# Kernel tuning notes

Hardware: AMD Instinct MI355X
Metric: run time of the kernel (lower is better)

## Reference

```python
import jax, jax.numpy as jnp
import numpy as np

B, T, IN_DIM, OUT_DIM = 1024, 64, 8, 2
H, K, HIDDEN = 3, 5, 256
LOG_STD_MIN, LOG_STD_MAX = -20.0, 2.0


def setup_inputs() -> dict:
    key = jax.random.key(0)
    ks = jax.random.split(key, 12)
    def lin(k, fan_in, fan_out):
        b = 1.0 / np.sqrt(fan_in)
        return jax.random.uniform(k, (fan_in, fan_out), jnp.float32, -b, b)
    inp = {
        'state': jax.random.normal(ks[0], (B, T, IN_DIM), jnp.float32),
        'noise': jax.random.normal(ks[1], (B, T, OUT_DIM), jnp.float32),
        'Wq': lin(ks[2], IN_DIM, K * H),
        'Wk': lin(ks[3], K, K * H),
        'Wv': lin(ks[4], K, K * H),
        'W1': lin(ks[5], K * H + IN_DIM, HIDDEN),
        'b1': jnp.zeros((HIDDEN,), jnp.float32),
        'W2': lin(ks[6], HIDDEN, HIDDEN),
        'b2': jnp.zeros((HIDDEN,), jnp.float32),
        'Wmu': jax.random.uniform(ks[7], (HIDDEN, OUT_DIM), jnp.float32, -0.003, 0.003),
        'bmu': jax.random.uniform(ks[8], (OUT_DIM,), jnp.float32, -0.003, 0.003),
        'Wls': jax.random.uniform(ks[9], (HIDDEN, OUT_DIM), jnp.float32, -0.003, 0.003),
        'bls': jax.random.uniform(ks[10], (OUT_DIM,), jnp.float32, -0.003, 0.003),
    }
    return inp


# static off-diagonal neighbor indices: row i -> all j != i
_OFFDIAG = np.array([[j for j in range(T) if j != i] for i in range(T)], dtype=np.int32)


def _forward(state, noise, Wq, Wk, Wv, W1, b1, W2, b2, Wmu, bmu, Wls, bls):
    b, t, _ = state.shape
    # rel[b,i,j] = state[b,j,:4] - state[b,i,:4]
    rel4 = state[:, None, :, 0:4] - state[:, :, None, 0:4]          # [b,t,t,4] (x,y,vx,vy)
    x_comp = rel4[..., 0::2]                                         # [x, vx]
    y_comp = rel4[..., 1::2]                                         # [y, vy]
    ang = (-state[:, :, 7] + 0.5 * jnp.pi)[:, None, :, None]         # varies with j (own-ref of key agent)
    c, s = jnp.cos(ang), jnp.sin(ang)
    xn = x_comp * c - y_comp * s                                     # [x', vx']
    yn = x_comp * s + y_comp * c                                     # [y', vy']
    rel = jnp.stack([xn[..., 0], yn[..., 0], xn[..., 1], yn[..., 1]], axis=-1)  # [b,t,t,4]
    # drop self-pairs (diagonal) -> [b,t,t-1,4]
    idx = jnp.asarray(_OFFDIAG)
    rel_od = rel[:, jnp.arange(t)[:, None], idx]
    r = jnp.sqrt(rel_od[..., 0] ** 2 + rel_od[..., 1] ** 2)[..., None]   # [b,t,t-1,1]
    r_trans = jax.nn.sigmoid(1.0 - 5.0 * (r - 0.2))                       # 1/(1+exp(-1+5(r-0.2)))
    rel_n = jnp.concatenate([rel_od[..., 0:2] / r, rel_od[..., 2:4], r_trans], axis=-1)  # [b,t,t-1,5]
    h, k = H, K
    q = (state @ Wq).reshape(b, t, h, k)                              # [b,t,h,k]
    keys = (rel_n @ Wk).reshape(b, t, t - 1, h, k)                    # [b,t,n,h,k]
    vals = (rel_n @ Wv).reshape(b, t, t - 1, h, k)
    scores = jnp.einsum('btnhk,bthk->bthn', keys, q) / jnp.sqrt(jnp.float32(k))
    w = jax.nn.softmax(scores, axis=-1)                               # over t-1 neighbors
    att = jnp.einsum('bthn,btnhk->bthk', w, vals).reshape(b, t, h * k)
    x = jnp.concatenate([att, state], axis=-1)
    x = jax.nn.relu(x @ W1 + b1)
    x = jax.nn.relu(x @ W2 + b2)
    mu = jnp.tanh(x @ Wmu + bmu)
    log_std = jnp.tanh(x @ Wls + bls)
    log_std = LOG_STD_MIN + 0.5 * (LOG_STD_MAX - LOG_STD_MIN) * (log_std + 1.0)
    std = jnp.exp(log_std)
    z = mu + std * noise                                              # rsample with explicit noise
    action = jnp.tanh(z)
    # Normal(mu,std).log_prob(z) with (z-mu)/std == noise
    log_prob = -0.5 * noise ** 2 - log_std - 0.5 * jnp.log(2.0 * jnp.pi)
    log_prob = log_prob - jnp.log(1.0 - action ** 2 + 1e-7)
    log_prob = jnp.sum(log_prob, axis=-1, keepdims=True)
    return action, log_prob


def reference(state, noise, Wq, Wk, Wv, W1, b1, W2, b2, Wmu, bmu, Wls, bls):
    return _forward(state, noise, Wq, Wk, Wv, W1, b1, W2, b2, Wmu, bmu, Wls, bls)
```

## Files before the change

### kernel.cpp

```cpp
#include <hip/hip_runtime.h>
#include <math.h>

#define NROWS 65536

typedef short bf16x8 __attribute__((ext_vector_type(8)));
typedef float f32x4  __attribute__((ext_vector_type(4)));
typedef float f32x2  __attribute__((ext_vector_type(2)));
typedef unsigned int u32x2 __attribute__((ext_vector_type(2)));

__device__ __forceinline__ unsigned short f2bf(float x){
    unsigned int u = __float_as_uint(x);
    u += 0x7FFFu + ((u >> 16) & 1u);
    return (unsigned short)(u >> 16);
}
__device__ __forceinline__ unsigned int pkbf(float lo, float hi){
    unsigned int r;
    asm("v_cvt_pk_bf16_f32 %0, %1, %2" : "=v"(r) : "v"(lo), "v"(hi));
    return r;
}
__device__ __forceinline__ f32x2 sp2(float x){ return (f32x2){x, x}; }

template<int CTRL, int RM>
__device__ __forceinline__ float dpp_add(float v){
    int m = __builtin_amdgcn_update_dpp(0, __float_as_int(v), CTRL, RM, 0xF, 1);
    return v + __int_as_float(m);
}
__device__ __forceinline__ float bfly8_add(float v){
    v = dpp_add<0xB1, 0xF>(v);
    v = dpp_add<0x4E, 0xF>(v);
    v = dpp_add<0x141, 0xF>(v);
    return v;
}
__device__ __forceinline__ float red4_lq(float v){
    v += __int_as_float(__builtin_amdgcn_ds_swizzle(__float_as_int(v), 0x401F));
    v += __shfl_xor(v, 32, 64);
    return v;
}
__device__ __forceinline__ float fast_tanh(float x){
    float e = __builtin_amdgcn_exp2f(x * 2.8853900817779268f);
    return 1.f - 2.f * __builtin_amdgcn_rcpf(e + 1.f);
}

__global__ __launch_bounds__(256) void prep_kernel(
    const float* __restrict__ W2, const float* __restrict__ W1,
    const float* __restrict__ Wq, const float* __restrict__ Wk,
    unsigned short* __restrict__ w2frag, unsigned short* __restrict__ w1frag,
    float* __restrict__ Cqk)
{
    const int bx = blockIdx.x, t = threadIdx.x;
    if (bx < 128){
        const int ct = bx >> 3, kk = bx & 7;
        #pragma unroll
        for (int s = 0; s < 2; ++s){
            int f = t * 2 + s;
            int lane = f >> 3, e = f & 7;
            int k = kk * 32 + (lane >> 4) * 8 + e;
            int c = ct * 16 + (lane & 15);
            w2frag[(size_t)(ct * 8 + kk) * 512 + f] = f2bf(W2[k * 256 + c]);
        }
    } else if (bx == 128){
        #pragma unroll
        for (int s = 0; s < 32; ++s){
            int flat = t * 32 + s;
            int ct = flat >> 9, r = flat & 511;
            int lane = r >> 3, e = r & 7;
            int k = (lane >> 4) * 8 + e;
            int c = ct * 16 + (lane & 15);
            w1frag[flat] = (k < 23) ? f2bf(W1[k * 256 + c]) : (unsigned short)0;
        }
    } else {
        if (t < 120){
            int h = t / 40, rem = t % 40, f = rem >> 3, d = rem & 7;
            float acc = 0.f;
            #pragma unroll
            for (int kk = 0; kk < 5; ++kk)
                acc += Wk[f * 15 + h * 5 + kk] * Wq[d * 15 + h * 5 + kk];
            Cqk[t] = acc * 0.64519834f;
        }
    }
}

__global__ __launch_bounds__(512, 4) void actor_kernel(
    const float* __restrict__ state, const float* __restrict__ noise,
    const float* __restrict__ Cqk,
    const float* __restrict__ Wv,
    const unsigned short* __restrict__ w1frag, const float* __restrict__ b1,
    const unsigned short* __restrict__ w2frag, const float* __restrict__ b2,
    const float* __restrict__ Wmu, const float* __restrict__ bmu,
    const float* __restrict__ Wls, const float* __restrict__ bls,
    float* __restrict__ action_out, float* __restrict__ logprob_out)
{
    __shared__ __align__(16) unsigned char uniA[64 * 264 * 2];
    float* sLDS  = (float*)uniA;
    float* pjLDS = sLDS + 576;
    float* qkLDS = pjLDS + 384;
    unsigned short* h1LDS = (unsigned short*)uniA;
    __shared__ __align__(16) unsigned short x0LDS[64 * 40];
    __shared__ __align__(16) float headLDS[8 * 64 * 4];

    const int t    = threadIdx.x;
    const int lane = t & 63;
    const int w    = t >> 6;
    const int lm   = lane & 15;
    const int lq   = lane >> 4;
    const int b    = blockIdx.x;

    {
        float v = state[(size_t)b * 512 + t];
        int r = t >> 3, c = t & 7;
        sLDS[r * 9 + c] = v;
        if (c < 4) pjLDS[(r & 31) * 12 + c * 2 + (r >> 5)] = v;

        if (t < 192){
            const int row = t & 63, h = t >> 6;
            f32x4 sA = *(const f32x4*)&state[(size_t)b * 512 + row * 8];
            f32x4 sB = *(const f32x4*)&state[(size_t)b * 512 + row * 8 + 4];
            #pragma unroll
            for (int f = 0; f < 5; ++f){
                const float* cp = &Cqk[(h * 5 + f) * 8];
                f32x4 cA = *(const f32x4*)cp;
                f32x4 cB = *(const f32x4*)(cp + 4);
                float acc = sA[0]*cA[0] + sA[1]*cA[1] + sA[2]*cA[2] + sA[3]*cA[3]
                          + sB[0]*cB[0] + sB[1]*cB[1] + sB[2]*cB[2] + sB[3]*cB[3];
                qkLDS[row * 20 + h * 5 + f] = acc;
            }
        } else if (w == 7){
            const int row = lane;
            float ang = 1.5707963267948966f - state[(size_t)b * 512 + row * 8 + 7];
            float sn, cs;
            __sincosf(ang, &sn, &cs);
            int base = (row & 31) * 12 + (row >> 5);
            pjLDS[base + 8]  = sn;
            pjLDS[base + 10] = cs;
        }
    }
    __syncthreads();

    {
        const int il = lane >> 3;
        const int js = lane & 7;
        const int i  = w * 8 + il;
        const float si0 = sLDS[i * 9 + 0], si1 = sLDS[i * 9 + 1];
        const float si2 = sLDS[i * 9 + 2], si3 = sLDS[i * 9 + 3];
        float qkv[16];
        *(f32x4*)&qkv[0]  = *(const f32x4*)&qkLDS[i * 20 + 0];
        *(f32x4*)&qkv[4]  = *(const f32x4*)&qkLDS[i * 20 + 4];
        *(f32x4*)&qkv[8]  = *(const f32x4*)&qkLDS[i * 20 + 8];
        *(f32x4*)&qkv[12] = *(const f32x4*)&qkLDS[i * 20 + 12];

        f32x2 s0 = {0.f,0.f}, s1 = {0.f,0.f}, s2 = {0.f,0.f};
        f32x2 g0[5], g1[5], g2[5];
        #pragma unroll
        for (int f = 0; f < 5; ++f){ g0[f] = sp2(0.f); g1[f] = sp2(0.f); g2[f] = sp2(0.f); }

        #pragma unroll
        for (int jj = 0; jj < 4; ++jj){
            const int jb = jj * 8 + js;
            const f32x2* pp = (const f32x2*)&pjLDS[jb * 12];
            f32x2 p0 = pp[0], p1 = pp[1], p2 = pp[2], p3 = pp[3];
            f32x2 sn = pp[4], cs = pp[5];
            f32x2 d0 = p0 - sp2(si0), d1 = p1 - sp2(si1);
            f32x2 d2 = p2 - sp2(si2), d3 = p3 - sp2(si3);
            f32x2 r2v = d0 * d0 + d1 * d1 + sp2(1e-30f);
            f32x2 xn0 = d0 * cs - d1 * sn, yn0 = d0 * sn + d1 * cs;
            f32x2 xn1 = d2 * cs - d3 * sn, yn1 = d2 * sn + d3 * cs;
            f32x2 inv_r;
            inv_r.x = __builtin_amdgcn_rsqf(r2v.x);
            inv_r.y = __builtin_amdgcn_rsqf(r2v.y);
            f32x2 rv  = r2v * inv_r;
            f32x2 arg = rv * sp2(7.2134752f) - sp2(2.8853901f);
            f32x2 f4;
            f4.x = __builtin_amdgcn_rcpf(1.f + __builtin_amdgcn_exp2f(arg.x));
            f4.y = __builtin_amdgcn_rcpf(1.f + __builtin_amdgcn_exp2f(arg.y));
            f32x2 f0 = xn0 * inv_r, f1 = yn0 * inv_r;
            f32x2 sc0 = f0*sp2(qkv[0])  + f1*sp2(qkv[1])  + xn1*sp2(qkv[2])  + yn1*sp2(qkv[3])  + f4*sp2(qkv[4]);
            f32x2 sc1 = f0*sp2(qkv[5])  + f1*sp2(qkv[6])  + xn1*sp2(qkv[7])  + yn1*sp2(qkv[8])  + f4*sp2(qkv[9]);
            f32x2 sc2 = f0*sp2(qkv[10]) + f1*sp2(qkv[11]) + xn1*sp2(qkv[12]) + yn1*sp2(qkv[13]) + f4*sp2(qkv[14]);
            f32x2 e0, e1, e2;
            e0.x = __builtin_amdgcn_exp2f(sc0.x);  e0.y = __builtin_amdgcn_exp2f(sc0.y);
            e1.x = __builtin_amdgcn_exp2f(sc1.x);  e1.y = __builtin_amdgcn_exp2f(sc1.y);
            e2.x = __builtin_amdgcn_exp2f(sc2.x);  e2.y = __builtin_amdgcn_exp2f(sc2.y);
            s0 += e0; s1 += e1; s2 += e2;
            g0[0] += e0*f0; g0[1] += e0*f1; g0[2] += e0*xn1; g0[3] += e0*yn1; g0[4] += e0*f4;
            g1[0] += e1*f0; g1[1] += e1*f1; g1[2] += e1*xn1; g1[3] += e1*yn1; g1[4] += e1*f4;
            g2[0] += e2*f0; g2[1] += e2*f1; g2[2] += e2*xn1; g2[3] += e2*yn1; g2[4] += e2*f4;
        }
        float S0 = s0.x + s0.y, S1 = s1.x + s1.y, S2 = s2.x + s2.y;
        float G0[5], G1[5], G2[5];
        #pragma unroll
        for (int f = 0; f < 5; ++f){
            G0[f] = bfly8_add(g0[f].x + g0[f].y);
            G1[f] = bfly8_add(g1[f].x + g1[f].y);
            G2[f] = bfly8_add(g2[f].x + g2[f].y);
        }
        S0 = bfly8_add(S0); S1 = bfly8_add(S1); S2 = bfly8_add(S2);

        {
            float argS = 7.2134752e-15f - 2.8853901f;
            float f4s  = __builtin_amdgcn_rcpf(1.f + __builtin_amdgcn_exp2f(argS));
            float es0 = __builtin_amdgcn_exp2f(f4s * qkv[4]);
            float es1 = __builtin_amdgcn_exp2f(f4s * qkv[9]);
            float es2 = __builtin_amdgcn_exp2f(f4s * qkv[14]);
            S0 -= es0; S1 -= es1; S2 -= es2;
            G0[4] -= es0 * f4s; G1[4] -= es1 * f4s; G2[4] -= es2 * f4s;
        }
        float i0 = __builtin_amdgcn_rcpf(S0);
        float i1 = __builtin_amdgcn_rcpf(S1);
        float i2 = __builtin_amdgcn_rcpf(S2);

        #pragma unroll
        for (int mm = 0; mm < 2; ++mm){
            int m = js * 2 + mm;
            if (m < 15){
                float A0 = (m < 5) ? G0[0] : (m < 10) ? G1[0] : G2[0];
                float A1 = (m < 5) ? G0[1] : (m < 10) ? G1[1] : G2[1];
                float A2 = (m < 5) ? G0[2] : (m < 10) ? G1[2] : G2[2];
                float A3 = (m < 5) ? G0[3] : (m < 10) ? G1[3] : G2[3];
                float A4 = (m < 5) ? G0[4] : (m < 10) ? G1[4] : G2[4];
                float I  = (m < 5) ? i0    : (m < 10) ? i1    : i2;
                float av = (A0 * Wv[m] + A1 * Wv[15 + m] + A2 * Wv[30 + m]
                          + A3 * Wv[45 + m] + A4 * Wv[60 + m]) * I;
                x0LDS[i * 40 + m] = f2bf(av);
            }
        }
        x0LDS[i * 40 + 15 + js] = f2bf(sLDS[i * 9 + js]);
        x0LDS[i * 40 + 23 + js] = 0;
        if (js == 0) x0LDS[i * 40 + 31] = 0;
    }
    __syncthreads();

    {
        bf16x8 afr[4];
        #pragma unroll
        for (int rt = 0; rt < 4; ++rt)
            afr[rt] = *(const bf16x8*)&x0LDS[(rt * 16 + lm) * 40 + lq * 8];
        #pragma unroll
        for (int ci = 0; ci < 2; ++ci){
            const int ct = w * 2 + ci;
            bf16x8 bfr = *(const bf16x8*)&w1frag[(size_t)ct * 512 + lane * 8];
            f32x4 bb = *(const f32x4*)&b1[ct * 16 + lq * 4];
            #pragma unroll
            for (int rt = 0; rt < 4; ++rt){
                f32x4 c0 = {0.f, 0.f, 0.f, 0.f};
                c0 = __builtin_amdgcn_mfma_f32_16x16x32_bf16(bfr, afr[rt], c0, 0, 0, 0);
                float h0 = fmaxf(c0[0] + bb[0], 0.f);
                float h1v = fmaxf(c0[1] + bb[1], 0.f);
                float h2v = fmaxf(c0[2] + bb[2], 0.f);
                float h3v = fmaxf(c0[3] + bb[3], 0.f);
                u32x2 pk; pk.x = pkbf(h0, h1v); pk.y = pkbf(h2v, h3v);
                *(u32x2*)&h1LDS[(rt * 16 + lm) * 264 + ct * 16 + lq * 4] = pk;
            }
        }
    }
    __syncthreads();

    {
        f32x4 acc[4][2];
        #pragma unroll
        for (int rt = 0; rt < 4; ++rt)
            #pragma unroll
            for (int ci = 0; ci < 2; ++ci) acc[rt][ci] = (f32x4){0.f, 0.f, 0.f, 0.f};

        #pragma unroll
        for (int kk = 0; kk < 8; ++kk){
            bf16x8 arf[4], brf[2];
            #pragma unroll
            for (int rt = 0; rt < 4; ++rt)
                arf[rt] = *(const bf16x8*)&h1LDS[(rt * 16 + lm) * 264 + kk * 32 + lq * 8];
            #pragma unroll
            for (int ci = 0; ci < 2; ++ci)
                brf[ci] = *(const bf16x8*)&w2frag[(size_t)((w * 2 + ci) * 8 + kk) * 512 + lane * 8];
            #pragma unroll
            for (int rt = 0; rt < 4; ++rt)
                #pragma unroll
                for (int ci = 0; ci < 2; ++ci)
                    acc[rt][ci] = __builtin_amdgcn_mfma_f32_16x16x32_bf16(brf[ci], arf[rt], acc[rt][ci], 0, 0, 0);
        }

        f32x4 b2v[2], wmA[2], wmB[2], wlA[2], wlB[2];
        #pragma unroll
        for (int ci = 0; ci < 2; ++ci){
            int cb = (w * 2 + ci) * 16 + lq * 4;
            b2v[ci] = *(const f32x4*)&b2[cb];
            wmA[ci] = *(const f32x4*)&Wmu[cb * 2];
            wmB[ci] = *(const f32x4*)&Wmu[cb * 2 + 4];
            wlA[ci] = *(const f32x4*)&Wls[cb * 2];
            wlB[ci] = *(const f32x4*)&Wls[cb * 2 + 4];
        }
        #pragma unroll
        for (int rt = 0; rt < 4; ++rt){
            float m0 = 0.f, m1 = 0.f, l0 = 0.f, l1 = 0.f;
            #pragma unroll
            for (int ci = 0; ci < 2; ++ci){
                float hv0 = fmaxf(acc[rt][ci][0] + b2v[ci][0], 0.f);
                float hv1 = fmaxf(acc[rt][ci][1] + b2v[ci][1], 0.f);
                float hv2 = fmaxf(acc[rt][ci][2] + b2v[ci][2], 0.f);
                float hv3 = fmaxf(acc[rt][ci][3] + b2v[ci][3], 0.f);
                m0 += hv0*wmA[ci][0] + hv1*wmA[ci][2] + hv2*wmB[ci][0] + hv3*wmB[ci][2];
                m1 += hv0*wmA[ci][1] + hv1*wmA[ci][3] + hv2*wmB[ci][1] + hv3*wmB[ci][3];
                l0 += hv0*wlA[ci][0] + hv1*wlA[ci][2] + hv2*wlB[ci][0] + hv3*wlB[ci][2];
                l1 += hv0*wlA[ci][1] + hv1*wlA[ci][3] + hv2*wlB[ci][1] + hv3*wlB[ci][3];
            }
            m0 = red4_lq(m0); m1 = red4_lq(m1);
            l0 = red4_lq(l0); l1 = red4_lq(l1);
            if (lq == 0){
                f32x4 o = {m0, m1, l0, l1};
                *(f32x4*)&headLDS[(w * 64 + rt * 16 + lm) * 4] = o;
            }
        }
    }
    __syncthreads();

    if (lane < 8){
        const int row = w * 8 + lane;
        f32x4 s = {0.f, 0.f, 0.f, 0.f};
        #pragma unroll
        for (int ww = 0; ww < 8; ++ww)
            s += *(const f32x4*)&headLDS[(ww * 64 + row) * 4];
        const size_t grow = (size_t)b * 64 + row;
        float2 nv = *(const float2*)&noise[grow * 2];
        float n0 = nv.x, n1 = nv.y;
        float lp = 0.f;
        {
            float mu = fast_tanh(s[0] + bmu[0]);
            float ls = fast_tanh(s[2] + bls[0]);
            ls = -20.f + 11.f * (ls + 1.f);
            float sd = __builtin_amdgcn_exp2f(ls * 1.4426950408889634f);
            float a = fast_tanh(mu + sd * n0);
            action_out[grow * 2 + 0] = a;
            lp += -0.5f * n0 * n0 - ls - 0.9189385332046727f
                - 0.6931471805599453f * __builtin_amdgcn_logf(1.f - a * a + 1e-7f);
        }
        {
            float mu = fast_tanh(s[1] + bmu[1]);
            float ls = fast_tanh(s[3] + bls[1]);
            ls = -20.f + 11.f * (ls + 1.f);
            float sd = __builtin_amdgcn_exp2f(ls * 1.4426950408889634f);
            float a = fast_tanh(mu + sd * n1);
            action_out[grow * 2 + 1] = a;
            lp += -0.5f * n1 * n1 - ls - 0.9189385332046727f
                - 0.6931471805599453f * __builtin_amdgcn_logf(1.f - a * a + 1e-7f);
        }
        logprob_out[grow] = lp;
    }
}

extern "C" void kernel_launch(void* const* d_in, const int* in_sizes, int n_in,
                              void* d_out, int out_size, void* d_ws, size_t ws_size,
                              hipStream_t stream)
{
    (void)in_sizes; (void)n_in; (void)out_size; (void)ws_size;
    const float* state = (const float*)d_in[0];
    const float* noise = (const float*)d_in[1];
    const float* Wq  = (const float*)d_in[2];
    const float* Wk  = (const float*)d_in[3];
    const float* Wv  = (const float*)d_in[4];
    const float* W1  = (const float*)d_in[5];
    const float* b1  = (const float*)d_in[6];
    const float* W2  = (const float*)d_in[7];
    const float* b2  = (const float*)d_in[8];
    const float* Wmu = (const float*)d_in[9];
    const float* bmu = (const float*)d_in[10];
    const float* Wls = (const float*)d_in[11];
    const float* bls = (const float*)d_in[12];

    unsigned short* w2frag = (unsigned short*)d_ws;
    unsigned short* w1frag = w2frag + 65536;
    float* Cqk = (float*)(w1frag + 8192);

    float* action_out  = (float*)d_out;
    float* logprob_out = (float*)d_out + (size_t)NROWS * 2;

    prep_kernel<<<130, 256, 0, stream>>>(W2, W1, Wq, Wk, w2frag, w1frag, Cqk);
    actor_kernel<<<1024, 512, 0, stream>>>(state, noise, Cqk, Wv,
        w1frag, b1, w2frag, b2, Wmu, bmu, Wls, bls, action_out, logprob_out);
}
```

Measured before the change: 111.6 us.

## Split each batch's 64 query rows across two 256-thread blocks

The actor kernel now launches two blocks per batch element, each handling 32 query rows with 4 waves instead of 64 rows with 8 waves. Each block still loads the full 64-agent state and trig projections, but computes attention, the MLP and the heads only for its half, with the MFMA tiling reshaped to 2 row tiles by 4 column tiles per wave. The intent is smaller blocks with less LDS, giving more resident blocks and better scheduling granularity. The cost is duplicated state loads, sin/cos and W2 fragment reads per batch, plus more barriers overall.

```diff
diff --git a/kernel.cpp b/kernel.cpp
--- a/kernel.cpp
+++ b/kernel.cpp
@@ -80,7 +80,7 @@
     }
 }
 
-__global__ __launch_bounds__(512, 4) void actor_kernel(
+__global__ __launch_bounds__(256, 4) void actor_kernel(
     const float* __restrict__ state, const float* __restrict__ noise,
     const float* __restrict__ Cqk,
     const float* __restrict__ Wv,
@@ -90,31 +90,38 @@
     const float* __restrict__ Wls, const float* __restrict__ bls,
     float* __restrict__ action_out, float* __restrict__ logprob_out)
 {
-    __shared__ __align__(16) unsigned char uniA[64 * 264 * 2];
+    __shared__ __align__(16) unsigned char uniA[32 * 264 * 2];
     float* sLDS  = (float*)uniA;
     float* pjLDS = sLDS + 576;
     float* qkLDS = pjLDS + 384;
     unsigned short* h1LDS = (unsigned short*)uniA;
-    __shared__ __align__(16) unsigned short x0LDS[64 * 40];
-    __shared__ __align__(16) float headLDS[8 * 64 * 4];
+    __shared__ __align__(16) unsigned short x0LDS[32 * 40];
+    __shared__ __align__(16) float headLDS[4 * 32 * 4];
 
     const int t    = threadIdx.x;
     const int lane = t & 63;
     const int w    = t >> 6;
     const int lm   = lane & 15;
     const int lq   = lane >> 4;
-    const int b    = blockIdx.x;
+    const int b    = blockIdx.x >> 1;
+    const int R0   = (blockIdx.x & 1) * 32;
 
     {
-        float v = state[(size_t)b * 512 + t];
+        const float* sb = &state[(size_t)b * 512];
+        float v0 = sb[t];
+        float v1 = sb[256 + t];
         int r = t >> 3, c = t & 7;
-        sLDS[r * 9 + c] = v;
-        if (c < 4) pjLDS[(r & 31) * 12 + c * 2 + (r >> 5)] = v;
-
-        if (t < 192){
-            const int row = t & 63, h = t >> 6;
-            f32x4 sA = *(const f32x4*)&state[(size_t)b * 512 + row * 8];
-            f32x4 sB = *(const f32x4*)&state[(size_t)b * 512 + row * 8 + 4];
+        sLDS[r * 9 + c] = v0;
+        sLDS[(r + 32) * 9 + c] = v1;
+        if (c < 4){
+            pjLDS[r * 12 + c * 2 + 0] = v0;
+            pjLDS[r * 12 + c * 2 + 1] = v1;
+        }
+        if (t < 96){
+            const int rl = t & 31, h = t >> 5;
+            const int row = R0 + rl;
+            f32x4 sA = *(const f32x4*)&sb[row * 8];
+            f32x4 sB = *(const f32x4*)&sb[row * 8 + 4];
             #pragma unroll
             for (int f = 0; f < 5; ++f){
                 const float* cp = &Cqk[(h * 5 + f) * 8];
@@ -122,14 +129,14 @@
                 f32x4 cB = *(const f32x4*)(cp + 4);
                 float acc = sA[0]*cA[0] + sA[1]*cA[1] + sA[2]*cA[2] + sA[3]*cA[3]
                           + sB[0]*cB[0] + sB[1]*cB[1] + sB[2]*cB[2] + sB[3]*cB[3];
-                qkLDS[row * 20 + h * 5 + f] = acc;
-            }
-        } else if (w == 7){
-            const int row = lane;
-            float ang = 1.5707963267948966f - state[(size_t)b * 512 + row * 8 + 7];
+                qkLDS[rl * 20 + h * 5 + f] = acc;
+            }
+        } else if (t >= 192){
+            const int j = t - 192;
+            float ang = 1.5707963267948966f - sb[j * 8 + 7];
             float sn, cs;
             __sincosf(ang, &sn, &cs);
-            int base = (row & 31) * 12 + (row >> 5);
+            int base = (j & 31) * 12 + (j >> 5);
             pjLDS[base + 8]  = sn;
             pjLDS[base + 10] = cs;
         }
@@ -139,14 +146,15 @@
     {
         const int il = lane >> 3;
         const int js = lane & 7;
-        const int i  = w * 8 + il;
+        const int iL = w * 8 + il;
+        const int i  = R0 + iL;
         const float si0 = sLDS[i * 9 + 0], si1 = sLDS[i * 9 + 1];
         const float si2 = sLDS[i * 9 + 2], si3 = sLDS[i * 9 + 3];
         float qkv[16];
-        *(f32x4*)&qkv[0]  = *(const f32x4*)&qkLDS[i * 20 + 0];
-        *(f32x4*)&qkv[4]  = *(const f32x4*)&qkLDS[i * 20 + 4];
-        *(f32x4*)&qkv[8]  = *(const f32x4*)&qkLDS[i * 20 + 8];
-        *(f32x4*)&qkv[12] = *(const f32x4*)&qkLDS[i * 20 + 12];
+        *(f32x4*)&qkv[0]  = *(const f32x4*)&qkLDS[iL * 20 + 0];
+        *(f32x4*)&qkv[4]  = *(const f32x4*)&qkLDS[iL * 20 + 4];
+        *(f32x4*)&qkv[8]  = *(const f32x4*)&qkLDS[iL * 20 + 8];
+        *(f32x4*)&qkv[12] = *(const f32x4*)&qkLDS[iL * 20 + 12];
 
         f32x2 s0 = {0.f,0.f}, s1 = {0.f,0.f}, s2 = {0.f,0.f};
         f32x2 g0[5], g1[5], g2[5];
@@ -220,27 +228,27 @@
                 float I  = (m < 5) ? i0    : (m < 10) ? i1    : i2;
                 float av = (A0 * Wv[m] + A1 * Wv[15 + m] + A2 * Wv[30 + m]
                           + A3 * Wv[45 + m] + A4 * Wv[60 + m]) * I;
-                x0LDS[i * 40 + m] = f2bf(av);
-            }
-        }
-        x0LDS[i * 40 + 15 + js] = f2bf(sLDS[i * 9 + js]);
-        x0LDS[i * 40 + 23 + js] = 0;
-        if (js == 0) x0LDS[i * 40 + 31] = 0;
+                x0LDS[iL * 40 + m] = f2bf(av);
+            }
+        }
+        x0LDS[iL * 40 + 15 + js] = f2bf(sLDS[i * 9 + js]);
+        x0LDS[iL * 40 + 23 + js] = 0;
+        if (js == 0) x0LDS[iL * 40 + 31] = 0;
     }
     __syncthreads();
 
     {
-        bf16x8 afr[4];
-        #pragma unroll
-        for (int rt = 0; rt < 4; ++rt)
+        bf16x8 afr[2];
+        #pragma unroll
+        for (int rt = 0; rt < 2; ++rt)
             afr[rt] = *(const bf16x8*)&x0LDS[(rt * 16 + lm) * 40 + lq * 8];
         #pragma unroll
-        for (int ci = 0; ci < 2; ++ci){
-            const int ct = w * 2 + ci;
+        for (int ci = 0; ci < 4; ++ci){
+            const int ct = w * 4 + ci;
             bf16x8 bfr = *(const bf16x8*)&w1frag[(size_t)ct * 512 + lane * 8];
             f32x4 bb = *(const f32x4*)&b1[ct * 16 + lq * 4];
             #pragma unroll
-            for (int rt = 0; rt < 4; ++rt){
+            for (int rt = 0; rt < 2; ++rt){
                 f32x4 c0 = {0.f, 0.f, 0.f, 0.f};
                 c0 = __builtin_amdgcn_mfma_f32_16x16x32_bf16(bfr, afr[rt], c0, 0, 0, 0);
                 float h0 = fmaxf(c0[0] + bb[0], 0.f);
@@ -255,69 +263,69 @@
     __syncthreads();
 
     {
-        f32x4 acc[4][2];
-        #pragma unroll
-        for (int rt = 0; rt < 4; ++rt)
-            #pragma unroll
-            for (int ci = 0; ci < 2; ++ci) acc[rt][ci] = (f32x4){0.f, 0.f, 0.f, 0.f};
+        f32x4 acc[2][4];
+        #pragma unroll
+        for (int rt = 0; rt < 2; ++rt)
+            #pragma unroll
+            for (int ci = 0; ci < 4; ++ci) acc[rt][ci] = (f32x4){0.f, 0.f, 0.f, 0.f};
 
         #pragma unroll
         for (int kk = 0; kk < 8; ++kk){
-            bf16x8 arf[4], brf[2];
-            #pragma unroll
-            for (int rt = 0; rt < 4; ++rt)
+            bf16x8 arf[2], brf[4];
+            #pragma unroll
+            for (int rt = 0; rt < 2; ++rt)
                 arf[rt] = *(const bf16x8*)&h1LDS[(rt * 16 + lm) * 264 + kk * 32 + lq * 8];
             #pragma unroll
-            for (int ci = 0; ci < 2; ++ci)
-                brf[ci] = *(const bf16x8*)&w2frag[(size_t)((w * 2 + ci) * 8 + kk) * 512 + lane * 8];
-            #pragma unroll
-            for (int rt = 0; rt < 4; ++rt)
+            for (int ci = 0; ci < 4; ++ci)
+                brf[ci] = *(const bf16x8*)&w2frag[(size_t)((w * 4 + ci) * 8 + kk) * 512 + lane * 8];
+            #pragma unroll
+            for (int rt = 0; rt < 2; ++rt)
                 #pragma unroll
-                for (int ci = 0; ci < 2; ++ci)
+                for (int ci = 0; ci < 4; ++ci)
                     acc[rt][ci] = __builtin_amdgcn_mfma_f32_16x16x32_bf16(brf[ci], arf[rt], acc[rt][ci], 0, 0, 0);
         }
 
-        f32x4 b2v[2], wmA[2], wmB[2], wlA[2], wlB[2];
-        #pragma unroll
-        for (int ci = 0; ci < 2; ++ci){
-            int cb = (w * 2 + ci) * 16 + lq * 4;
-            b2v[ci] = *(const f32x4*)&b2[cb];
-            wmA[ci] = *(const f32x4*)&Wmu[cb * 2];
-            wmB[ci] = *(const f32x4*)&Wmu[cb * 2 + 4];
-            wlA[ci] = *(const f32x4*)&Wls[cb * 2];
-            wlB[ci] = *(const f32x4*)&Wls[cb * 2 + 4];
-        }
-        #pragma unroll
-        for (int rt = 0; rt < 4; ++rt){
-            float m0 = 0.f, m1 = 0.f, l0 = 0.f, l1 = 0.f;
-            #pragma unroll
-            for (int ci = 0; ci < 2; ++ci){
-                float hv0 = fmaxf(acc[rt][ci][0] + b2v[ci][0], 0.f);
-                float hv1 = fmaxf(acc[rt][ci][1] + b2v[ci][1], 0.f);
-                float hv2 = fmaxf(acc[rt][ci][2] + b2v[ci][2], 0.f);
-                float hv3 = fmaxf(acc[rt][ci][3] + b2v[ci][3], 0.f);
-                m0 += hv0*wmA[ci][0] + hv1*wmA[ci][2] + hv2*wmB[ci][0] + hv3*wmB[ci][2];
-                m1 += hv0*wmA[ci][1] + hv1*wmA[ci][3] + hv2*wmB[ci][1] + hv3*wmB[ci][3];
-                l0 += hv0*wlA[ci][0] + hv1*wlA[ci][2] + hv2*wlB[ci][0] + hv3*wlB[ci][2];
-                l1 += hv0*wlA[ci][1] + hv1*wlA[ci][3] + hv2*wlB[ci][1] + hv3*wlB[ci][3];
-            }
-            m0 = red4_lq(m0); m1 = red4_lq(m1);
-            l0 = red4_lq(l0); l1 = red4_lq(l1);
+        float m0[2] = {0.f, 0.f}, m1[2] = {0.f, 0.f};
+        float l0[2] = {0.f, 0.f}, l1[2] = {0.f, 0.f};
+        #pragma unroll
+        for (int ci = 0; ci < 4; ++ci){
+            int cb = (w * 4 + ci) * 16 + lq * 4;
+            f32x4 b2v = *(const f32x4*)&b2[cb];
+            f32x4 wmA = *(const f32x4*)&Wmu[cb * 2];
+            f32x4 wmB = *(const f32x4*)&Wmu[cb * 2 + 4];
+            f32x4 wlA = *(const f32x4*)&Wls[cb * 2];
+            f32x4 wlB = *(const f32x4*)&Wls[cb * 2 + 4];
+            #pragma unroll
+            for (int rt = 0; rt < 2; ++rt){
+                float hv0 = fmaxf(acc[rt][ci][0] + b2v[0], 0.f);
+                float hv1 = fmaxf(acc[rt][ci][1] + b2v[1], 0.f);
+                float hv2 = fmaxf(acc[rt][ci][2] + b2v[2], 0.f);
+                float hv3 = fmaxf(acc[rt][ci][3] + b2v[3], 0.f);
+                m0[rt] += hv0*wmA[0] + hv1*wmA[2] + hv2*wmB[0] + hv3*wmB[2];
+                m1[rt] += hv0*wmA[1] + hv1*wmA[3] + hv2*wmB[1] + hv3*wmB[3];
+                l0[rt] += hv0*wlA[0] + hv1*wlA[2] + hv2*wlB[0] + hv3*wlB[2];
+                l1[rt] += hv0*wlA[1] + hv1*wlA[3] + hv2*wlB[1] + hv3*wlB[3];
+            }
+        }
+        #pragma unroll
+        for (int rt = 0; rt < 2; ++rt){
+            float a0 = red4_lq(m0[rt]), a1 = red4_lq(m1[rt]);
+            float a2 = red4_lq(l0[rt]), a3 = red4_lq(l1[rt]);
             if (lq == 0){
-                f32x4 o = {m0, m1, l0, l1};
-                *(f32x4*)&headLDS[(w * 64 + rt * 16 + lm) * 4] = o;
+                f32x4 o = {a0, a1, a2, a3};
+                *(f32x4*)&headLDS[(w * 32 + rt * 16 + lm) * 4] = o;
             }
         }
     }
     __syncthreads();
 
     if (lane < 8){
-        const int row = w * 8 + lane;
+        const int rowL = w * 8 + lane;
         f32x4 s = {0.f, 0.f, 0.f, 0.f};
         #pragma unroll
-        for (int ww = 0; ww < 8; ++ww)
-            s += *(const f32x4*)&headLDS[(ww * 64 + row) * 4];
-        const size_t grow = (size_t)b * 64 + row;
+        for (int ww = 0; ww < 4; ++ww)
+            s += *(const f32x4*)&headLDS[(ww * 32 + rowL) * 4];
+        const size_t grow = (size_t)b * 64 + R0 + rowL;
         float2 nv = *(const float2*)&noise[grow * 2];
         float n0 = nv.x, n1 = nv.y;
         float lp = 0.f;
@@ -372,6 +380,6 @@
     float* logprob_out = (float*)d_out + (size_t)NROWS * 2;
 
     prep_kernel<<<130, 256, 0, stream>>>(W2, W1, Wq, Wk, w2frag, w1frag, Cqk);
-    actor_kernel<<<1024, 512, 0, stream>>>(state, noise, Cqk, Wv,
+    actor_kernel<<<2048, 256, 0, stream>>>(state, noise, Cqk, Wv,
         w1frag, b1, w2frag, b2, Wmu, bmu, Wls, bls, action_out, logprob_out);
 }
```

Result: slower. 114.0 us (+2.2%).

## Prefetch W2 fragments into registers before the barrier and stage prep transpose via LDS

Applied to the files above, without the earlier changes.

The main kernel now loads all sixteen W2 bf16 fragments per wave from global memory into registers before the barrier that precedes the layer-1 MFMA stage, so their latency overlaps with the attention/layer-1 work instead of stalling the layer-2 MFMA loop. The state columns of x0 are written during the initial state load rather than in the attention loop. The prep kernel coalesces W2 reads through a shared-memory tile before scattering into fragment order. This costs 64 extra VGPRs per thread held across the layer-1 stage, which risks lowering occupancy or causing spills.

```diff
diff --git a/kernel.cpp b/kernel.cpp
--- a/kernel.cpp
+++ b/kernel.cpp
@@ -49,14 +49,22 @@
 {
     const int bx = blockIdx.x, t = threadIdx.x;
     if (bx < 128){
+        __shared__ float tile[512];
         const int ct = bx >> 3, kk = bx & 7;
+        #pragma unroll
+        for (int s = 0; s < 2; ++s){
+            int flat = t * 2 + s;
+            int kl = flat >> 4, cl = flat & 15;
+            tile[flat] = W2[(kk * 32 + kl) * 256 + ct * 16 + cl];
+        }
+        __syncthreads();
         #pragma unroll
         for (int s = 0; s < 2; ++s){
             int f = t * 2 + s;
             int lane = f >> 3, e = f & 7;
-            int k = kk * 32 + (lane >> 4) * 8 + e;
-            int c = ct * 16 + (lane & 15);
-            w2frag[(size_t)(ct * 8 + kk) * 512 + f] = f2bf(W2[k * 256 + c]);
+            int kl = (lane >> 4) * 8 + e;
+            int cl = lane & 15;
+            w2frag[(size_t)(ct * 8 + kk) * 512 + f] = f2bf(tile[kl * 16 + cl]);
         }
     } else if (bx == 128){
         #pragma unroll
@@ -110,11 +118,15 @@
         int r = t >> 3, c = t & 7;
         sLDS[r * 9 + c] = v;
         if (c < 4) pjLDS[(r & 31) * 12 + c * 2 + (r >> 5)] = v;
+        x0LDS[r * 40 + 15 + c] = f2bf(v);
+        x0LDS[r * 40 + 23 + c] = 0;
+        if (c == 0) x0LDS[r * 40 + 31] = 0;
 
         if (t < 192){
             const int row = t & 63, h = t >> 6;
-            f32x4 sA = *(const f32x4*)&state[(size_t)b * 512 + row * 8];
-            f32x4 sB = *(const f32x4*)&state[(size_t)b * 512 + row * 8 + 4];
+            const float* sb = &state[(size_t)b * 512];
+            f32x4 sA = *(const f32x4*)&sb[row * 8];
+            f32x4 sB = *(const f32x4*)&sb[row * 8 + 4];
             #pragma unroll
             for (int f = 0; f < 5; ++f){
                 const float* cp = &Cqk[(h * 5 + f) * 8];
@@ -223,10 +235,16 @@
                 x0LDS[i * 40 + m] = f2bf(av);
             }
         }
-        x0LDS[i * 40 + 15 + js] = f2bf(sLDS[i * 9 + js]);
-        x0LDS[i * 40 + 23 + js] = 0;
-        if (js == 0) x0LDS[i * 40 + 31] = 0;
-    }
+    }
+
+    bf16x8 brfp[16];
+    #pragma unroll
+    for (int q = 0; q < 16; ++q){
+        int ci = q >> 3, kk = q & 7;
+        brfp[q] = *(const bf16x8*)&w2frag[(size_t)((w * 2 + ci) * 8 + kk) * 512 + lane * 8];
+    }
+    __builtin_amdgcn_sched_barrier(0);
+
     __syncthreads();
 
     {
@@ -263,18 +281,15 @@
 
         #pragma unroll
         for (int kk = 0; kk < 8; ++kk){
-            bf16x8 arf[4], brf[2];
+            bf16x8 arf[4];
             #pragma unroll
             for (int rt = 0; rt < 4; ++rt)
                 arf[rt] = *(const bf16x8*)&h1LDS[(rt * 16 + lm) * 264 + kk * 32 + lq * 8];
-            #pragma unroll
-            for (int ci = 0; ci < 2; ++ci)
-                brf[ci] = *(const bf16x8*)&w2frag[(size_t)((w * 2 + ci) * 8 + kk) * 512 + lane * 8];
             #pragma unroll
             for (int rt = 0; rt < 4; ++rt)
                 #pragma unroll
                 for (int ci = 0; ci < 2; ++ci)
-                    acc[rt][ci] = __builtin_amdgcn_mfma_f32_16x16x32_bf16(brf[ci], arf[rt], acc[rt][ci], 0, 0, 0);
+                    acc[rt][ci] = __builtin_amdgcn_mfma_f32_16x16x32_bf16(brfp[ci * 8 + kk], arf[rt], acc[rt][ci], 0, 0, 0);
         }
 
         f32x4 b2v[2], wmA[2], wmB[2], wlA[2], wlB[2];
```

Measured after the change: 111.1 us, median of 2. Within noise of the previous version (-0.4%).
